# Kernel tuning notes

Measured on AMD Instinct MI355X. Metric: run time of the kernel, lower is better.

## Reference

```python
import jax, jax.numpy as jnp
import numpy as np

B, S, L, F = 32, 48, 64, 256


def setup_inputs() -> dict:
    key = jax.random.key(0)
    ks = jax.random.split(key, 7)
    return {
        "features": jax.random.normal(ks[0], (B, S, L, F), dtype=jnp.float32),
        "src_locs": jax.random.normal(ks[1], (B, L, 2), dtype=jnp.float32),
        "tar_locs": jax.random.normal(ks[2], (B, 2), dtype=jnp.float32),
        "W1": jax.random.normal(ks[3], (F, F), dtype=jnp.float32) * (1.0 / np.sqrt(F)),
        "b1": jax.random.normal(ks[4], (F,), dtype=jnp.float32) * 0.02,
        "W2": jax.random.normal(ks[5], (F, 1), dtype=jnp.float32) * (1.0 / np.sqrt(F)),
        "b2": jax.random.normal(ks[6], (1,), dtype=jnp.float32) * 0.02,
    }


def reference(features, src_locs, tar_locs, W1, b1, W2, b2):
    # features: (B, S, L, F); src_locs: (B, L, 2); tar_locs: (B, 2)
    # MLP score: Linear(F,F) + ReLU + Linear(F,1) + ReLU -> (B, S, L, 1)
    attn = jax.nn.relu(jnp.einsum('bslf,fg->bslg', features, W1) + b1)
    attn = jax.nn.relu(jnp.einsum('bslf,fo->bslo', attn, W2) + b2)  # (B,S,L,1)
    # inverse-distance weights over stations: (B, L)
    dists = jnp.sqrt(jnp.sum((src_locs - tar_locs[:, None, :]) ** 2, axis=-1))
    inv_dists = 1.0 / dists  # (B, L)
    # broadcast to (B, 1, L, 1), softmax over src_length axis (axis=2)
    attn_scores = jax.nn.softmax(attn * inv_dists[:, None, :, None], axis=2)
    # weighted sum over stations -> (B, S, F)
    return jnp.sum(features * attn_scores, axis=2)
```

## Files before the change

kernel.cpp:

```cpp
#include <hip/hip_runtime.h>
#include <hip/hip_fp16.h>
#include <math.h>

typedef _Float16 half8 __attribute__((ext_vector_type(8)));
typedef float floatx4 __attribute__((ext_vector_type(4)));

#define BB 32
#define SS 48
#define LL 64
#define FF 256

__global__ __launch_bounds__(256) void prep_w(const float* __restrict__ W1,
                                              _Float16* __restrict__ whi,
                                              _Float16* __restrict__ wlo) {
    int idx = blockIdx.x * 256 + threadIdx.x;
    int j    = idx & 7;
    int lane = (idx >> 3) & 63;
    int nt   = (idx >> 9) & 15;
    int kt   = idx >> 13;
    int k = kt * 32 + ((lane >> 4) & 3) * 8 + j;
    int n = nt * 16 + (lane & 15);
    float x = W1[k * FF + n];
    _Float16 hi = (_Float16)x;
    _Float16 lo = (_Float16)(x - (float)hi);
    whi[idx] = hi;
    wlo[idx] = lo;
}

__global__ __launch_bounds__(256, 2) void ida_mfma(
    const float* __restrict__ features,
    const float* __restrict__ src_locs,
    const float* __restrict__ tar_locs,
    const _Float16* __restrict__ whi,
    const _Float16* __restrict__ wlo,
    const float* __restrict__ b1,
    const float* __restrict__ W2,
    const float* __restrict__ b2,
    float* __restrict__ out)
{
    __shared__ _Float16 Ahi[8192];
    __shared__ _Float16 Alo[8192];
    __shared__ float SP[LL * 4];
    __shared__ float wbuf[LL];
    __shared__ float red[4 * FF];

    const int t    = threadIdx.x;
    const int w    = t >> 6;
    const int lane = t & 63;
    const int quad = lane >> 4;
    const int l16  = lane & 15;
    const int bs   = blockIdx.x;
    const int b    = bs / SS;

    const float* Xg = features + (size_t)bs * (LL * FF);

    floatx4 acc[4][4] = {};
    half8 bh[4][4], bl[4][4];

    #pragma unroll
    for (int ktl = 0; ktl < 4; ++ktl)
        #pragma unroll
        for (int nt = 0; nt < 4; ++nt) {
            size_t off = ((size_t)(ktl * 16 + w * 4 + nt) * 64 + lane) * 8;
            bh[ktl][nt] = *((const half8*)(whi + off));
            bl[ktl][nt] = *((const half8*)(wlo + off));
        }

    for (int kh = 0; kh < 2; ++kh) {
        __syncthreads();
        for (int ktl = 0; ktl < 4; ++ktl) {
            int kt = kh * 4 + ktl;
            const float4* p = (const float4*)(Xg + (w * 16 + l16) * FF + kt * 32 + quad * 8);
            float4 x0 = p[0], x1 = p[1];
            float xs[8] = {x0.x, x0.y, x0.z, x0.w, x1.x, x1.y, x1.z, x1.w};
            half8 hi, lo;
            #pragma unroll
            for (int j = 0; j < 8; ++j) {
                _Float16 h = (_Float16)xs[j];
                hi[j] = h;
                lo[j] = (_Float16)(xs[j] - (float)h);
            }
            *((half8*)&Ahi[((w * 4 + ktl) * 64 + lane) * 8]) = hi;
            *((half8*)&Alo[((w * 4 + ktl) * 64 + lane) * 8]) = lo;
        }
        __syncthreads();

        #pragma unroll
        for (int ktl = 0; ktl < 4; ++ktl) {
            #pragma unroll
            for (int mt = 0; mt < 4; ++mt) {
                half8 ahi = *((half8*)&Ahi[((mt * 4 + ktl) * 64 + lane) * 8]);
                half8 alo = *((half8*)&Alo[((mt * 4 + ktl) * 64 + lane) * 8]);
                #pragma unroll
                for (int nt = 0; nt < 4; ++nt) {
                    acc[mt][nt] = __builtin_amdgcn_mfma_f32_16x16x32_f16(ahi, bh[ktl][nt], acc[mt][nt], 0, 0, 0);
                    acc[mt][nt] = __builtin_amdgcn_mfma_f32_16x16x32_f16(ahi, bl[ktl][nt], acc[mt][nt], 0, 0, 0);
                    acc[mt][nt] = __builtin_amdgcn_mfma_f32_16x16x32_f16(alo, bh[ktl][nt], acc[mt][nt], 0, 0, 0);
                }
            }
        }

        if (kh == 0) {
            #pragma unroll
            for (int ktl = 0; ktl < 4; ++ktl)
                #pragma unroll
                for (int nt = 0; nt < 4; ++nt) {
                    size_t off = ((size_t)((4 + ktl) * 16 + w * 4 + nt) * 64 + lane) * 8;
                    bh[ktl][nt] = *((const half8*)(whi + off));
                    bl[ktl][nt] = *((const half8*)(wlo + off));
                }
        }
    }

    float b1v[4], w2v[4];
    #pragma unroll
    for (int nt = 0; nt < 4; ++nt) {
        int n = (w * 4 + nt) * 16 + l16;
        b1v[nt] = b1[n];
        w2v[nt] = W2[n];
    }
    #pragma unroll
    for (int mt = 0; mt < 4; ++mt) {
        #pragma unroll
        for (int r = 0; r < 4; ++r) {
            float p = 0.f;
            #pragma unroll
            for (int nt = 0; nt < 4; ++nt) {
                float h = fmaxf(acc[mt][nt][r] + b1v[nt], 0.f);
                p = fmaf(h, w2v[nt], p);
            }
            p += __shfl_xor(p, 1);
            p += __shfl_xor(p, 2);
            p += __shfl_xor(p, 4);
            p += __shfl_xor(p, 8);
            if (l16 == 0) SP[(mt * 16 + quad * 4 + r) * 4 + w] = p;
        }
    }
    __syncthreads();

    if (t < LL) {
        float s = SP[4 * t] + SP[4 * t + 1] + SP[4 * t + 2] + SP[4 * t + 3] + b2[0];
        float score = fmaxf(s, 0.f);
        float dx = src_locs[(b * LL + t) * 2 + 0] - tar_locs[b * 2 + 0];
        float dy = src_locs[(b * LL + t) * 2 + 1] - tar_locs[b * 2 + 1];
        float inv = 1.0f / sqrtf(dx * dx + dy * dy);
        float logit = score * inv;
        float m = logit;
        #pragma unroll
        for (int o = 32; o > 0; o >>= 1) m = fmaxf(m, __shfl_xor(m, o));
        float e = __expf(logit - m);
        float se = e;
        #pragma unroll
        for (int o = 32; o > 0; o >>= 1) se += __shfl_xor(se, o);
        wbuf[t] = e / se;
    }
    __syncthreads();

    {
        const float4* Xg4 = (const float4*)Xg;
        floatx4 o = {0.f, 0.f, 0.f, 0.f};
        #pragma unroll
        for (int lr = 0; lr < 16; ++lr) {
            int l = w * 16 + lr;
            float wl = wbuf[l];
            float4 x = Xg4[l * 64 + lane];
            o[0] = fmaf(x.x, wl, o[0]);
            o[1] = fmaf(x.y, wl, o[1]);
            o[2] = fmaf(x.z, wl, o[2]);
            o[3] = fmaf(x.w, wl, o[3]);
        }
        #pragma unroll
        for (int j = 0; j < 4; ++j)
            red[w * FF + lane * 4 + j] = o[j];
    }
    __syncthreads();
    {
        float o = red[0 * FF + t] + red[1 * FF + t] + red[2 * FF + t] + red[3 * FF + t];
        out[bs * FF + t] = o;
    }
}

extern "C" void kernel_launch(void* const* d_in, const int* in_sizes, int n_in,
                              void* d_out, int out_size, void* d_ws, size_t ws_size,
                              hipStream_t stream) {
    const float* features = (const float*)d_in[0];
    const float* src_locs = (const float*)d_in[1];
    const float* tar_locs = (const float*)d_in[2];
    const float* W1       = (const float*)d_in[3];
    const float* b1       = (const float*)d_in[4];
    const float* W2       = (const float*)d_in[5];
    const float* b2       = (const float*)d_in[6];
    float* out = (float*)d_out;

    _Float16* whi = (_Float16*)d_ws;
    _Float16* wlo = whi + FF * FF;

    prep_w<<<dim3(FF * FF / 256), dim3(256), 0, stream>>>(W1, whi, wlo);
    ida_mfma<<<dim3(BB * SS), dim3(256), 0, stream>>>(
        features, src_locs, tar_locs, whi, wlo, b1, W2, b2, out);
}
```

Measured before the change: 182.6 us.

## Process two (b,s) rows per block to amortize W1 fragment loads

Each block now handles 128 feature rows (two batch-sequence pairs) instead of 64, so each W1 hi/lo fragment loaded from global memory feeds twice as many MFMAs. W1 fragments are now loaded per k-tile inside the loop rather than held for a whole half of K. The A staging buffers double to 64KB of LDS, and the small reduction buffers are aliased onto that space. The grid is halved, which lowers occupancy and parallelism, and the larger accumulator array raises register pressure.

After: 202.1 us. 1.11x slower.

```diff
diff --git a/kernel.cpp b/kernel.cpp
--- a/kernel.cpp
+++ b/kernel.cpp
@@ -38,79 +38,71 @@
     const float* __restrict__ b2,
     float* __restrict__ out)
 {
-    __shared__ _Float16 Ahi[8192];
-    __shared__ _Float16 Alo[8192];
-    __shared__ float SP[LL * 4];
-    __shared__ float wbuf[LL];
-    __shared__ float red[4 * FF];
+    __shared__ _Float16 Ahi[16384];
+    __shared__ _Float16 Alo[16384];
 
     const int t    = threadIdx.x;
     const int w    = t >> 6;
     const int lane = t & 63;
     const int quad = lane >> 4;
     const int l16  = lane & 15;
-    const int bs   = blockIdx.x;
-    const int b    = bs / SS;
+    const int blk  = blockIdx.x;
 
-    const float* Xg = features + (size_t)bs * (LL * FF);
+    const float* Xg = features + (size_t)blk * 128 * FF;
 
-    floatx4 acc[4][4] = {};
-    half8 bh[4][4], bl[4][4];
-
-    #pragma unroll
-    for (int ktl = 0; ktl < 4; ++ktl)
-        #pragma unroll
-        for (int nt = 0; nt < 4; ++nt) {
-            size_t off = ((size_t)(ktl * 16 + w * 4 + nt) * 64 + lane) * 8;
-            bh[ktl][nt] = *((const half8*)(whi + off));
-            bl[ktl][nt] = *((const half8*)(wlo + off));
-        }
+    floatx4 acc[8][4] = {};
 
     for (int kh = 0; kh < 2; ++kh) {
         __syncthreads();
-        for (int ktl = 0; ktl < 4; ++ktl) {
-            int kt = kh * 4 + ktl;
-            const float4* p = (const float4*)(Xg + (w * 16 + l16) * FF + kt * 32 + quad * 8);
-            float4 x0 = p[0], x1 = p[1];
-            float xs[8] = {x0.x, x0.y, x0.z, x0.w, x1.x, x1.y, x1.z, x1.w};
-            half8 hi, lo;
+        #pragma unroll
+        for (int rg = 0; rg < 2; ++rg) {
+            const int mtg = 2 * w + rg;
             #pragma unroll
-            for (int j = 0; j < 8; ++j) {
-                _Float16 h = (_Float16)xs[j];
-                hi[j] = h;
-                lo[j] = (_Float16)(xs[j] - (float)h);
+            for (int ktl = 0; ktl < 4; ++ktl) {
+                const float4* p = (const float4*)(Xg + (mtg * 16 + l16) * FF + kh * 128 + ktl * 32 + quad * 8);
+                float4 x0 = p[0], x1 = p[1];
+                float xs[8] = {x0.x, x0.y, x0.z, x0.w, x1.x, x1.y, x1.z, x1.w};
+                half8 hi, lo;
+                #pragma unroll
+                for (int j = 0; j < 8; ++j) {
+                    _Float16 h = (_Float16)xs[j];
+                    hi[j] = h;
+                    lo[j] = (_Float16)(xs[j] - (float)h);
+                }
+                *((half8*)&Ahi[((mtg * 4 + ktl) * 64 + lane) * 8]) = hi;
+                *((half8*)&Alo[((mtg * 4 + ktl) * 64 + lane) * 8]) = lo;
             }
-            *((half8*)&Ahi[((w * 4 + ktl) * 64 + lane) * 8]) = hi;
-            *((half8*)&Alo[((w * 4 + ktl) * 64 + lane) * 8]) = lo;
         }
         __syncthreads();
 
         #pragma unroll
         for (int ktl = 0; ktl < 4; ++ktl) {
+            const int kt = kh * 4 + ktl;
+            half8 bh[4], bl[4];
             #pragma unroll
-            for (int mt = 0; mt < 4; ++mt) {
+            for (int nt = 0; nt < 4; ++nt) {
+                size_t off = ((size_t)(kt * 16 + w * 4 + nt) * 64 + lane) * 8;
+                bh[nt] = *((const half8*)(whi + off));
+                bl[nt] = *((const half8*)(wlo + off));
+            }
+            #pragma unroll
+            for (int mt = 0; mt < 8; ++mt) {
                 half8 ahi = *((half8*)&Ahi[((mt * 4 + ktl) * 64 + lane) * 8]);
                 half8 alo = *((half8*)&Alo[((mt * 4 + ktl) * 64 + lane) * 8]);
                 #pragma unroll
                 for (int nt = 0; nt < 4; ++nt) {
-                    acc[mt][nt] = __builtin_amdgcn_mfma_f32_16x16x32_f16(ahi, bh[ktl][nt], acc[mt][nt], 0, 0, 0);
-                    acc[mt][nt] = __builtin_amdgcn_mfma_f32_16x16x32_f16(ahi, bl[ktl][nt], acc[mt][nt], 0, 0, 0);
-                    acc[mt][nt] = __builtin_amdgcn_mfma_f32_16x16x32_f16(alo, bh[ktl][nt], acc[mt][nt], 0, 0, 0);
+                    acc[mt][nt] = __builtin_amdgcn_mfma_f32_16x16x32_f16(ahi, bh[nt], acc[mt][nt], 0, 0, 0);
+                    acc[mt][nt] = __builtin_amdgcn_mfma_f32_16x16x32_f16(ahi, bl[nt], acc[mt][nt], 0, 0, 0);
+                    acc[mt][nt] = __builtin_amdgcn_mfma_f32_16x16x32_f16(alo, bh[nt], acc[mt][nt], 0, 0, 0);
                 }
             }
         }
+    }
+    __syncthreads();
 
-        if (kh == 0) {
-            #pragma unroll
-            for (int ktl = 0; ktl < 4; ++ktl)
-                #pragma unroll
-                for (int nt = 0; nt < 4; ++nt) {
-                    size_t off = ((size_t)((4 + ktl) * 16 + w * 4 + nt) * 64 + lane) * 8;
-                    bh[ktl][nt] = *((const half8*)(whi + off));
-                    bl[ktl][nt] = *((const half8*)(wlo + off));
-                }
-        }
-    }
+    float* SP   = (float*)Ahi;
+    float* wbuf = SP + 512;
+    float* red  = wbuf + 128;
 
     float b1v[4], w2v[4];
     #pragma unroll
@@ -120,7 +112,7 @@
         w2v[nt] = W2[n];
     }
     #pragma unroll
-    for (int mt = 0; mt < 4; ++mt) {
+    for (int mt = 0; mt < 8; ++mt) {
         #pragma unroll
         for (int r = 0; r < 4; ++r) {
             float p = 0.f;
@@ -138,11 +130,15 @@
     }
     __syncthreads();
 
-    if (t < LL) {
+    if (t < 128) {
+        const int g   = t >> 6;
+        const int l   = t & 63;
+        const int bsg = blk * 2 + g;
+        const int b   = bsg / SS;
         float s = SP[4 * t] + SP[4 * t + 1] + SP[4 * t + 2] + SP[4 * t + 3] + b2[0];
         float score = fmaxf(s, 0.f);
-        float dx = src_locs[(b * LL + t) * 2 + 0] - tar_locs[b * 2 + 0];
-        float dy = src_locs[(b * LL + t) * 2 + 1] - tar_locs[b * 2 + 1];
+        float dx = src_locs[(b * LL + l) * 2 + 0] - tar_locs[b * 2 + 0];
+        float dy = src_locs[(b * LL + l) * 2 + 1] - tar_locs[b * 2 + 1];
         float inv = 1.0f / sqrtf(dx * dx + dy * dy);
         float logit = score * inv;
         float m = logit;
@@ -160,10 +156,10 @@
         const float4* Xg4 = (const float4*)Xg;
         floatx4 o = {0.f, 0.f, 0.f, 0.f};
         #pragma unroll
-        for (int lr = 0; lr < 16; ++lr) {
-            int l = w * 16 + lr;
-            float wl = wbuf[l];
-            float4 x = Xg4[l * 64 + lane];
+        for (int lr = 0; lr < 32; ++lr) {
+            int r = 32 * w + lr;
+            float wl = wbuf[r];
+            float4 x = Xg4[r * 64 + lane];
             o[0] = fmaf(x.x, wl, o[0]);
             o[1] = fmaf(x.y, wl, o[1]);
             o[2] = fmaf(x.z, wl, o[2]);
@@ -175,8 +171,10 @@
     }
     __syncthreads();
     {
-        float o = red[0 * FF + t] + red[1 * FF + t] + red[2 * FF + t] + red[3 * FF + t];
-        out[bs * FF + t] = o;
+        float o0 = red[0 * FF + t] + red[1 * FF + t];
+        float o1 = red[2 * FF + t] + red[3 * FF + t];
+        out[(size_t)(blk * 2 + 0) * FF + t] = o0;
+        out[(size_t)(blk * 2 + 1) * FF + t] = o1;
     }
 }
 
@@ -196,6 +194,6 @@
     _Float16* wlo = whi + FF * FF;
 
     prep_w<<<dim3(FF * FF / 256), dim3(256), 0, stream>>>(W1, whi, wlo);
-    ida_mfma<<<dim3(BB * SS), dim3(256), 0, stream>>>(
+    ida_mfma<<<dim3(BB * SS / 2), dim3(256), 0, stream>>>(
         features, src_locs, tar_locs, whi, wlo, b1, W2, b2, out);
 }
```

## Split fused kernel into score and finalize kernels and stream W1 fragments per k-tile

Applied to the files above, without the earlier changes.

Splits the monolithic kernel into a score kernel that writes logits to workspace and a separate finalize kernel doing the softmax and weighted feature sum. The score kernel no longer keeps all W1 fragments in registers; it loads them per k-tile, and its launch bound asks for 4 blocks per SIMD instead of 2 to raise occupancy. prep_w now reads W1 coalesced and scatters into the fragment layout. The cost is reading the features tensor twice across two kernels (the second read may hit cache), an extra launch, and more global or L2 traffic for W1 fragments inside the inner loop.

Measured after the change: 191.7 us. +5.0%, slower.

```diff
diff --git a/kernel.cpp b/kernel.cpp
--- a/kernel.cpp
+++ b/kernel.cpp
@@ -14,20 +14,18 @@
                                               _Float16* __restrict__ whi,
                                               _Float16* __restrict__ wlo) {
     int idx = blockIdx.x * 256 + threadIdx.x;
-    int j    = idx & 7;
-    int lane = (idx >> 3) & 63;
-    int nt   = (idx >> 9) & 15;
-    int kt   = idx >> 13;
-    int k = kt * 32 + ((lane >> 4) & 3) * 8 + j;
-    int n = nt * 16 + (lane & 15);
-    float x = W1[k * FF + n];
+    float x = W1[idx];
+    int k = idx >> 8, n = idx & 255;
+    int kt = k >> 5, quad = (k >> 3) & 3, j = k & 7;
+    int nt = n >> 4, l16 = n & 15;
+    int lane = quad * 16 + l16;
+    size_t off = ((size_t)(kt * 16 + nt) * 64 + lane) * 8 + j;
     _Float16 hi = (_Float16)x;
-    _Float16 lo = (_Float16)(x - (float)hi);
-    whi[idx] = hi;
-    wlo[idx] = lo;
-}
-
-__global__ __launch_bounds__(256, 2) void ida_mfma(
+    whi[off] = hi;
+    wlo[off] = (_Float16)(x - (float)hi);
+}
+
+__global__ __launch_bounds__(256, 4) void ida_scores(
     const float* __restrict__ features,
     const float* __restrict__ src_locs,
     const float* __restrict__ tar_locs,
@@ -36,13 +34,11 @@
     const float* __restrict__ b1,
     const float* __restrict__ W2,
     const float* __restrict__ b2,
-    float* __restrict__ out)
+    float* __restrict__ logits)
 {
     __shared__ _Float16 Ahi[8192];
     __shared__ _Float16 Alo[8192];
     __shared__ float SP[LL * 4];
-    __shared__ float wbuf[LL];
-    __shared__ float red[4 * FF];
 
     const int t    = threadIdx.x;
     const int w    = t >> 6;
@@ -55,16 +51,6 @@
     const float* Xg = features + (size_t)bs * (LL * FF);
 
     floatx4 acc[4][4] = {};
-    half8 bh[4][4], bl[4][4];
-
-    #pragma unroll
-    for (int ktl = 0; ktl < 4; ++ktl)
-        #pragma unroll
-        for (int nt = 0; nt < 4; ++nt) {
-            size_t off = ((size_t)(ktl * 16 + w * 4 + nt) * 64 + lane) * 8;
-            bh[ktl][nt] = *((const half8*)(whi + off));
-            bl[ktl][nt] = *((const half8*)(wlo + off));
-        }
 
     for (int kh = 0; kh < 2; ++kh) {
         __syncthreads();
@@ -87,28 +73,25 @@
 
         #pragma unroll
         for (int ktl = 0; ktl < 4; ++ktl) {
+            const int kt = kh * 4 + ktl;
+            half8 bh[4], bl[4];
+            #pragma unroll
+            for (int nt = 0; nt < 4; ++nt) {
+                size_t off = ((size_t)(kt * 16 + w * 4 + nt) * 64 + lane) * 8;
+                bh[nt] = *((const half8*)(whi + off));
+                bl[nt] = *((const half8*)(wlo + off));
+            }
             #pragma unroll
             for (int mt = 0; mt < 4; ++mt) {
                 half8 ahi = *((half8*)&Ahi[((mt * 4 + ktl) * 64 + lane) * 8]);
                 half8 alo = *((half8*)&Alo[((mt * 4 + ktl) * 64 + lane) * 8]);
                 #pragma unroll
                 for (int nt = 0; nt < 4; ++nt) {
-                    acc[mt][nt] = __builtin_amdgcn_mfma_f32_16x16x32_f16(ahi, bh[ktl][nt], acc[mt][nt], 0, 0, 0);
-                    acc[mt][nt] = __builtin_amdgcn_mfma_f32_16x16x32_f16(ahi, bl[ktl][nt], acc[mt][nt], 0, 0, 0);
-                    acc[mt][nt] = __builtin_amdgcn_mfma_f32_16x16x32_f16(alo, bh[ktl][nt], acc[mt][nt], 0, 0, 0);
+                    acc[mt][nt] = __builtin_amdgcn_mfma_f32_16x16x32_f16(ahi, bh[nt], acc[mt][nt], 0, 0, 0);
+                    acc[mt][nt] = __builtin_amdgcn_mfma_f32_16x16x32_f16(ahi, bl[nt], acc[mt][nt], 0, 0, 0);
+                    acc[mt][nt] = __builtin_amdgcn_mfma_f32_16x16x32_f16(alo, bh[nt], acc[mt][nt], 0, 0, 0);
                 }
             }
-        }
-
-        if (kh == 0) {
-            #pragma unroll
-            for (int ktl = 0; ktl < 4; ++ktl)
-                #pragma unroll
-                for (int nt = 0; nt < 4; ++nt) {
-                    size_t off = ((size_t)((4 + ktl) * 16 + w * 4 + nt) * 64 + lane) * 8;
-                    bh[ktl][nt] = *((const half8*)(whi + off));
-                    bl[ktl][nt] = *((const half8*)(wlo + off));
-                }
         }
     }
 
@@ -144,7 +127,27 @@
         float dx = src_locs[(b * LL + t) * 2 + 0] - tar_locs[b * 2 + 0];
         float dy = src_locs[(b * LL + t) * 2 + 1] - tar_locs[b * 2 + 1];
         float inv = 1.0f / sqrtf(dx * dx + dy * dy);
-        float logit = score * inv;
+        logits[(size_t)bs * LL + t] = score * inv;
+    }
+}
+
+__global__ __launch_bounds__(256) void ida_finalize(
+    const float* __restrict__ features,
+    const float* __restrict__ logits,
+    float* __restrict__ out)
+{
+    __shared__ float wbuf[LL];
+    __shared__ float red[4 * FF];
+
+    const int t    = threadIdx.x;
+    const int w    = t >> 6;
+    const int lane = t & 63;
+    const int bs   = blockIdx.x;
+
+    const float* Xg = features + (size_t)bs * (LL * FF);
+
+    if (t < LL) {
+        float logit = logits[(size_t)bs * LL + t];
         float m = logit;
         #pragma unroll
         for (int o = 32; o > 0; o >>= 1) m = fmaxf(m, __shfl_xor(m, o));
@@ -176,7 +179,7 @@
     __syncthreads();
     {
         float o = red[0 * FF + t] + red[1 * FF + t] + red[2 * FF + t] + red[3 * FF + t];
-        out[bs * FF + t] = o;
+        out[(size_t)bs * FF + t] = o;
     }
 }
 
@@ -192,10 +195,12 @@
     const float* b2       = (const float*)d_in[6];
     float* out = (float*)d_out;
 
-    _Float16* whi = (_Float16*)d_ws;
-    _Float16* wlo = whi + FF * FF;
+    _Float16* whi  = (_Float16*)d_ws;
+    _Float16* wlo  = whi + FF * FF;
+    float* logits  = (float*)(wlo + FF * FF);
 
     prep_w<<<dim3(FF * FF / 256), dim3(256), 0, stream>>>(W1, whi, wlo);
-    ida_mfma<<<dim3(BB * SS), dim3(256), 0, stream>>>(
-        features, src_locs, tar_locs, whi, wlo, b1, W2, b2, out);
-}
+    ida_scores<<<dim3(BB * SS), dim3(256), 0, stream>>>(
+        features, src_locs, tar_locs, whi, wlo, b1, W2, b2, logits);
+    ida_finalize<<<dim3(BB * SS), dim3(256), 0, stream>>>(features, logits, out);
+}
```
